# Kernel tuning notes

Measured on AMD Instinct MI355X. Metric: run time of the kernel, lower is better.

Reference implementation:

```python
import jax, jax.numpy as jnp
import numpy as np

B, L, D_MODEL, N_HEADS = 2, 2048, 2048, 16
HEAD_DIM = D_MODEL // N_HEADS
EPS = 1e-6
ROPE_THETA = 10000.0


def rms_norm(x, scale):
    # normalize over head_dim, learnable per-dim scale (QKNorm)
    var = jnp.mean(jnp.square(x), axis=-1, keepdims=True)
    return x * jax.lax.rsqrt(var + EPS) * scale


def rope(x, offset=0):
    # x: [B, H, T, D]; rotate-half rotary embedding over flattened positions
    T, D = x.shape[-2], x.shape[-1]
    half = D // 2
    inv_freq = 1.0 / (ROPE_THETA ** (jnp.arange(0, half, dtype=jnp.float32) / half))
    pos = jnp.arange(T, dtype=jnp.float32) + offset
    ang = pos[:, None] * inv_freq[None, :]            # [T, half]
    cos, sin = jnp.cos(ang), jnp.sin(ang)
    x1, x2 = x[..., :half], x[..., half:]
    return jnp.concatenate([x1 * cos - x2 * sin, x1 * sin + x2 * cos], axis=-1)


def setup_inputs() -> dict:
    key = jax.random.key(0)
    ks = jax.random.split(key, 7)
    s = 1.0 / np.sqrt(D_MODEL)
    x = jax.random.normal(ks[0], (B, L, D_MODEL), dtype=jnp.float32)
    w_qkv = jax.random.uniform(ks[1], (D_MODEL, 3 * D_MODEL), jnp.float32, -s, s)
    b_qkv = jax.random.uniform(ks[2], (3 * D_MODEL,), jnp.float32, -s, s)
    q_scale = jnp.ones((HEAD_DIM,), jnp.float32)
    k_scale = jnp.ones((HEAD_DIM,), jnp.float32)
    w_out = jax.random.uniform(ks[3], (D_MODEL, D_MODEL), jnp.float32, -s, s)
    b_out = jax.random.uniform(ks[4], (D_MODEL,), jnp.float32, -s, s)
    mask = jnp.tril(jnp.ones((L, L), dtype=bool))   # causal block mask pattern
    return {"x": x, "w_qkv": w_qkv, "b_qkv": b_qkv, "q_scale": q_scale,
            "k_scale": k_scale, "w_out": w_out, "b_out": b_out, "mask": mask}


def reference(x, w_qkv, b_qkv, q_scale, k_scale, w_out, b_out, mask):
    b, t, _ = x.shape
    qkv = x @ w_qkv + b_qkv                                   # [B, T, 3*D]
    qkv = qkv.reshape(b, t, 3, N_HEADS, HEAD_DIM)
    q, k, v = jnp.moveaxis(qkv, 2, 0)                          # each [B, T, H, D]
    q = jnp.transpose(q, (0, 2, 1, 3))                         # [B, H, T, D]
    k = jnp.transpose(k, (0, 2, 1, 3))
    v = jnp.transpose(v, (0, 2, 1, 3))
    q = rms_norm(q, q_scale)
    k = rms_norm(k, k_scale)
    q = rope(q, offset=0)
    k = rope(k, offset=0)
    scores = jnp.einsum('bhqd,bhkd->bhqk', q, k) / np.sqrt(HEAD_DIM)
    scores = jnp.where(mask[None, None, :, :], scores, jnp.float32(-1e30))
    attn = jax.nn.softmax(scores, axis=-1)
    out = jnp.einsum('bhqk,bhkd->bhqd', attn, v)               # [B, H, T, D]
    out = jnp.transpose(out, (0, 2, 1, 3)).reshape(b, t, D_MODEL)
    return out @ w_out + b_out
```

## Files before the change

### kernel.cpp

```cpp
#include <hip/hip_runtime.h>
#include <hip/hip_bf16.h>
#include <stdint.h>


typedef unsigned short ushort8 __attribute__((ext_vector_type(8)));
typedef unsigned short ushort4v __attribute__((ext_vector_type(4)));
typedef short          bf16x8 __attribute__((ext_vector_type(8)));
typedef float          f32x4  __attribute__((ext_vector_type(4)));

#define B_   2
#define L_   2048
#define DM   2048
#define NH   16
#define HD   128
#define QKW  4096

__device__ __forceinline__ uint16_t f2bf(float f){
  uint32_t u = __builtin_bit_cast(uint32_t, f);
  u += 0x7FFFu + ((u >> 16) & 1u);
  return (uint16_t)(u >> 16);
}
__device__ __forceinline__ float bf2f(uint16_t h){
  uint32_t u = ((uint32_t)h) << 16;
  return __builtin_bit_cast(float, u);
}

#define GLD16(gp, lp) __builtin_amdgcn_global_load_lds( \
  (const __attribute__((address_space(1))) void*)(gp),  \
  (__attribute__((address_space(3))) void*)(lp), 16, 0, 0)

__global__ __launch_bounds__(256) void rope_table(float* __restrict__ ct, float* __restrict__ st){
  int i = blockIdx.x * 256 + threadIdx.x;
  int t = i >> 6, d = i & 63;
  float invf = powf(10000.f, -(float)d * (1.f/64.f));
  float s, c;
  sincosf((float)t * invf, &s, &c);
  ct[i] = c; st[i] = s;
}

__global__ __launch_bounds__(256) void cvt_f32_bf16(const float* __restrict__ x,
                                                    uint16_t* __restrict__ o, int n8){
  int i = blockIdx.x * 256 + threadIdx.x;
  if (i < n8){
    const float4* xv = (const float4*)x;
    float4 a = xv[(size_t)i*2], b = xv[(size_t)i*2+1];
    ushort8 v;
    v[0]=f2bf(a.x); v[1]=f2bf(a.y); v[2]=f2bf(a.z); v[3]=f2bf(a.w);
    v[4]=f2bf(b.x); v[5]=f2bf(b.y); v[6]=f2bf(b.z); v[7]=f2bf(b.w);
    *(ushort8*)(o + (size_t)i*8) = v;
  }
}

__global__ __launch_bounds__(256) void transpose_w(const float* __restrict__ W,
                                                   uint16_t* __restrict__ Wt, int R, int C){
  __shared__ float T[64][65];
  const int rb = blockIdx.x, cb = blockIdx.y;
  const int tid = threadIdx.x;
#pragma unroll
  for (int i=0;i<4;i++){
    int rr = i*16 + (tid >> 4);
    int cc = (tid & 15) * 4;
    float4 v = *(const float4*)(W + (size_t)(rb*64 + rr) * C + cb*64 + cc);
    T[rr][cc] = v.x; T[rr][cc+1] = v.y; T[rr][cc+2] = v.z; T[rr][cc+3] = v.w;
  }
  __syncthreads();
  const int oc = tid >> 2, rc = (tid & 3) * 16;
  ushort8 o0, o1;
#pragma unroll
  for (int j=0;j<8;j++){ o0[j] = f2bf(T[rc+j][oc]); o1[j] = f2bf(T[rc+8+j][oc]); }
  size_t ob = (size_t)(cb*64 + oc) * R + rb*64 + rc;
  *(ushort8*)(Wt + ob)     = o0;
  *(ushort8*)(Wt + ob + 8) = o1;
}

template<int MODE>
__global__ __launch_bounds__(512, 2) void gemm8p(
    const uint16_t* __restrict__ A, const uint16_t* __restrict__ Bt,
    const float* __restrict__ bias, void* __restrict__ Cv, void* __restrict__ Cv2,
    int M, int N, int K, int nbn, int ldc,
    const float* __restrict__ qs, const float* __restrict__ ks,
    const float* __restrict__ ct, const float* __restrict__ st)
{
  __shared__ uint16_t LA[3*16384];
  __shared__ uint16_t LB[3*8192];
  __shared__ float sums[4][2][64];
  const int nwg = (M >> 8) * nbn;
  const int q8  = nwg >> 3;
  const int id  = ((int)blockIdx.x & 7) * q8 + ((int)blockIdx.x >> 3);
  const int bm = id / nbn, bn = id % nbn;
  const int tid = threadIdx.x;
  const int lane = tid & 63, w = tid >> 6;
  const int wm = w & 3, wn = w >> 2;
  const int l15 = lane & 15, lh = lane >> 4;
  const int NT = K >> 6;

  const int qs3 = ((lane & 7) ^ ((lane >> 3) & 7)) * 8;
  const uint16_t* gA_ = A  + (size_t)((bm << 8) + (w << 5) + (lane >> 3)) * K + qs3;
  const uint16_t* gB_ = Bt + (size_t)((bn << 7) + (w << 4) + (lane >> 3)) * K + qs3;
  uint16_t* lA_ = LA + (w << 11);
  uint16_t* lB_ = LB + (w << 10);

  const int sw0 = ((lh       ^ (l15 & 7)) << 3);
  const int sw1 = (((4 | lh) ^ (l15 & 7)) << 3);
  const int aoff = (((wm << 6) + l15) << 6);
  const int boff = (((wn << 5) + l15) << 6);
  const int bno[4] = {0, 1024, 4096, 5120};

  f32x4 acc[4][4];
#pragma unroll
  for (int i=0;i<4;i++)
#pragma unroll
    for (int j=0;j<4;j++) acc[i][j] = f32x4{0.f,0.f,0.f,0.f};

  auto STAGE_A = [&](int tt, int s, int i){
    GLD16(gA_ + (size_t)tt*64 + (size_t)(i*8)*K, lA_ + s*16384 + i*512);
  };
  auto STAGE_B = [&](int tt, int s, int i){
    GLD16(gB_ + (size_t)tt*64 + (size_t)(i*8)*K, lB_ + s*8192 + i*512);
  };

#pragma unroll
  for (int i=0;i<4;i++) STAGE_A(0, 0, i);
#pragma unroll
  for (int i=0;i<2;i++) STAGE_B(0, 0, i);
#pragma unroll
  for (int i=0;i<4;i++) STAGE_A(1, 1, i);
#pragma unroll
  for (int i=0;i<2;i++) STAGE_B(1, 1, i);
  asm volatile("s_waitcnt vmcnt(6)" ::: "memory");
  __builtin_amdgcn_s_barrier();

  int sl = 0, sl2 = 2;
  for (int t = 0; t < NT; ++t){
    const bool pf = (t + 2 < NT);
    const uint16_t* la = LA + sl*16384;
    const uint16_t* lb = LB + sl*8192;

    bf16x8 af0[4], bf0[4], af1[4], bf1[4];
#pragma unroll
    for (int mi=0;mi<4;mi++) af0[mi] = *(const bf16x8*)(la + aoff + mi*1024 + sw0);
#pragma unroll
    for (int ni=0;ni<4;ni++) bf0[ni] = *(const bf16x8*)(lb + boff + bno[ni] + sw0);
#pragma unroll
    for (int mi=0;mi<4;mi++) af1[mi] = *(const bf16x8*)(la + aoff + mi*1024 + sw1);
#pragma unroll
    for (int ni=0;ni<4;ni++) bf1[ni] = *(const bf16x8*)(lb + boff + bno[ni] + sw1);
    if (pf){
      STAGE_A(t+2, sl2, 0); STAGE_A(t+2, sl2, 1);
      STAGE_A(t+2, sl2, 2); STAGE_A(t+2, sl2, 3);
      STAGE_B(t+2, sl2, 0); STAGE_B(t+2, sl2, 1);
    }
    __builtin_amdgcn_s_setprio(1);
#pragma unroll
    for (int mi=0;mi<4;mi++)
#pragma unroll
      for (int ni=0;ni<4;ni++)
        acc[mi][ni] = __builtin_amdgcn_mfma_f32_16x16x32_bf16(af0[mi], bf0[ni], acc[mi][ni], 0, 0, 0);
#pragma unroll
    for (int mi=0;mi<4;mi++)
#pragma unroll
      for (int ni=0;ni<4;ni++)
        acc[mi][ni] = __builtin_amdgcn_mfma_f32_16x16x32_bf16(af1[mi], bf1[ni], acc[mi][ni], 0, 0, 0);
    __builtin_amdgcn_s_setprio(0);

    if (t < NT-2)       { asm volatile("s_waitcnt vmcnt(6)" ::: "memory"); }
    else if (t == NT-2) { asm volatile("s_waitcnt vmcnt(0)" ::: "memory"); }
    if (t < NT-1) __builtin_amdgcn_s_barrier();
    sl  = (sl  == 2) ? 0 : sl  + 1;
    sl2 = (sl2 == 2) ? 0 : sl2 + 1;
  }

  const int cm = (bm << 8) + (wm << 6);
  const int cn = (bn << 7);
  int dc[4];
#pragma unroll
  for (int ni=0;ni<4;ni++) dc[ni] = (wn<<5) + ((ni>>1)<<6) + ((ni&1)<<4) + l15;
  float bs[4];
#pragma unroll
  for (int ni=0;ni<4;ni++) bs[ni] = bias[cn + dc[ni]];

  if (MODE == 0){
#pragma unroll
    for (int mi=0;mi<4;mi++)
#pragma unroll
      for (int r=0;r<4;r++){
        int rowg = cm + mi*16 + lh*4 + r;
#pragma unroll
        for (int ni=0;ni<4;ni++)
          ((float*)Cv)[(size_t)rowg * ldc + cn + dc[ni]] = acc[mi][ni][r] + bs[ni];
      }
  } else {
    const int part = bn >> 4;
    if (part == 2){
      uint16_t* vtp = (uint16_t*)Cv2;
      const int h  = bn & 15;
      const int bb = cm >> 11;
      const int t0 = (cm & (L_-1)) + lh*4;
#pragma unroll
      for (int mi=0;mi<4;mi++){
#pragma unroll
        for (int ni=0;ni<4;ni++){
          ushort4v pk;
#pragma unroll
          for (int r=0;r<4;r++) pk[r] = f2bf(acc[mi][ni][r] + bs[ni]);
          *(ushort4v*)(vtp + ((size_t)((bb*16 + h)*128 + dc[ni]))*L_ + t0 + mi*16) = pk;
        }
      }
    } else {
      uint16_t* Cb = (uint16_t*)Cv;
      const float* scp = part ? ks : qs;
      float scv[4];
#pragma unroll
      for (int ni=0;ni<4;ni++) scv[ni] = scp[dc[ni]];
      float ssum[4][4];
#pragma unroll
      for (int mi=0;mi<4;mi++)
#pragma unroll
        for (int r=0;r<4;r++){
          float s = 0.f;
#pragma unroll
          for (int ni=0;ni<4;ni++){
            float v = acc[mi][ni][r] + bs[ni];
            acc[mi][ni][r] = v;
            s += v*v;
          }
          s += __shfl_xor(s, 1); s += __shfl_xor(s, 2);
          s += __shfl_xor(s, 4); s += __shfl_xor(s, 8);
          ssum[mi][r] = s;
        }
      if (l15 == 0){
#pragma unroll
        for (int mi=0;mi<4;mi++)
#pragma unroll
          for (int r=0;r<4;r++) sums[wm][wn][mi*16 + lh*4 + r] = ssum[mi][r];
      }
      __syncthreads();
      const int dd0 = (wn<<5) + l15, dd1 = dd0 + 16;
#pragma unroll
      for (int mi=0;mi<4;mi++){
#pragma unroll
        for (int r=0;r<4;r++){
          int rid = mi*16 + lh*4 + r;
          float tot = ssum[mi][r] + sums[wm][wn^1][rid];
          float iv = rsqrtf(tot * 0.0078125f + 1e-6f);
          int rowg = cm + rid;
          int t = rowg & (L_-1);
          float y0 = acc[mi][0][r] * iv * scv[0];
          float y1 = acc[mi][1][r] * iv * scv[1];
          float y2 = acc[mi][2][r] * iv * scv[2];
          float y3 = acc[mi][3][r] * iv * scv[3];
          float c0 = ct[t*64 + dd0], s0 = st[t*64 + dd0];
          float c1 = ct[t*64 + dd1], s1 = st[t*64 + dd1];
          size_t rb_ = (size_t)rowg * ldc + cn;
          Cb[rb_ + dc[0]] = f2bf(y0*c0 - y2*s0);
          Cb[rb_ + dc[1]] = f2bf(y1*c1 - y3*s1);
          Cb[rb_ + dc[2]] = f2bf(y0*s0 + y2*c0);
          Cb[rb_ + dc[3]] = f2bf(y1*s1 + y3*c1);
        }
      }
    }
  }
}

__global__ __launch_bounds__(256) void flash_attn(
    const uint16_t* __restrict__ qk, const uint16_t* __restrict__ vt,
    uint16_t* __restrict__ ao)
{
  const int qp = blockIdx.x;
  const int bh = blockIdx.y;
  const int b = bh >> 4, h = bh & 15;
  const int tid = threadIdx.x;
  const int lane = tid & 63, w = tid >> 6;
  const int l15 = lane & 15, lh = lane >> 4;

  __shared__ uint16_t Ks[64][136];
  __shared__ uint16_t Vs[128][72];
  __shared__ uint16_t Ps[4][16][72];

  const float SCL = 0.12751744f;

  for (int sel = 0; sel < 2; sel++){
    const int qb = sel ? (31 - qp) : qp;

    const size_t qrow = (size_t)b * L_ + qb*64 + w*16 + l15;
    const uint16_t* qp_ = qk + qrow * QKW + h * HD;
    bf16x8 qf[4];
#pragma unroll
    for (int c = 0; c < 4; c++) qf[c] = *(const bf16x8*)(qp_ + c*32 + lh*8);

    float m_s = -3.0e38f, l_s = 0.f;
    f32x4 oacc[8];
#pragma unroll
    for (int nt = 0; nt < 8; nt++) oacc[nt] = f32x4{0.f,0.f,0.f,0.f};

    const int ntile = qb + 1;
    ushort8 rk[4], rv[4];

#pragma unroll
    for (int i = 0; i < 4; i++){
      int g = i*256 + tid, row = g >> 4, c = g & 15;
      rk[i] = *(const ushort8*)(qk + ((size_t)b*L_ + row)*QKW + DM + h*HD + c*8);
    }
#pragma unroll
    for (int i = 0; i < 4; i++){
      int g = i*256 + tid, d = g >> 3, c = g & 7;
      rv[i] = *(const ushort8*)(vt + ((size_t)bh*HD + d)*L_ + c*8);
    }

    for (int kt = 0; kt < ntile; kt++){
      __syncthreads();
#pragma unroll
      for (int i = 0; i < 4; i++){ int g = i*256+tid; *(ushort8*)(&Ks[g>>4][(g&15)*8]) = rk[i]; }
#pragma unroll
      for (int i = 0; i < 4; i++){ int g = i*256+tid; *(ushort8*)(&Vs[g>>3][(g&7)*8]) = rv[i]; }
      __syncthreads();

      if (kt + 1 < ntile){
        const int k2 = (kt + 1) * 64;
#pragma unroll
        for (int i = 0; i < 4; i++){
          int g = i*256 + tid, row = g >> 4, c = g & 15;
          rk[i] = *(const ushort8*)(qk + ((size_t)b*L_ + k2 + row)*QKW + DM + h*HD + c*8);
        }
#pragma unroll
        for (int i = 0; i < 4; i++){
          int g = i*256 + tid, d = g >> 3, c = g & 7;
          rv[i] = *(const ushort8*)(vt + ((size_t)bh*HD + d)*L_ + k2 + c*8);
        }
      }

      f32x4 s[4];
#pragma unroll
      for (int nt = 0; nt < 4; nt++) s[nt] = f32x4{0.f,0.f,0.f,0.f};
      __builtin_amdgcn_s_setprio(1);
#pragma unroll
      for (int c = 0; c < 4; c++){
#pragma unroll
        for (int nt = 0; nt < 4; nt++){
          bf16x8 kf = *(const bf16x8*)(&Ks[nt*16 + l15][c*32 + lh*8]);
          s[nt] = __builtin_amdgcn_mfma_f32_16x16x32_bf16(kf, qf[c], s[nt], 0, 0, 0);
        }
      }
      __builtin_amdgcn_s_setprio(0);

      const bool diag = (kt == qb);
      const int qg = w*16 + l15;
      const int kb = lh*4;
#pragma unroll
      for (int nt = 0; nt < 4; nt++){
#pragma unroll
        for (int r = 0; r < 4; r++){
          float v = s[nt][r] * SCL;
          if (diag && (nt*16 + kb + r > qg)) v = -1.0e30f;
          s[nt][r] = v;
        }
      }
      float pm = s[0][0];
#pragma unroll
      for (int nt = 0; nt < 4; nt++)
#pragma unroll
        for (int r = 0; r < 4; r++) pm = fmaxf(pm, s[nt][r]);
      pm = fmaxf(pm, __shfl_xor(pm, 16));
      pm = fmaxf(pm, __shfl_xor(pm, 32));
      if (!__all(pm - m_s <= 8.0f)){
        float mn = fmaxf(m_s, pm);
        float alpha = exp2f(m_s - mn);
        m_s = mn; l_s *= alpha;
        float ar[4];
#pragma unroll
        for (int r = 0; r < 4; r++) ar[r] = __shfl(alpha, lh*4 + r);
#pragma unroll
        for (int nt = 0; nt < 8; nt++)
#pragma unroll
          for (int r = 0; r < 4; r++) oacc[nt][r] *= ar[r];
      }
      float rs = 0.f;
#pragma unroll
      for (int nt = 0; nt < 4; nt++){
        float p0 = exp2f(s[nt][0] - m_s);
        float p1 = exp2f(s[nt][1] - m_s);
        float p2 = exp2f(s[nt][2] - m_s);
        float p3 = exp2f(s[nt][3] - m_s);
        rs += (p0 + p1) + (p2 + p3);
        uint2 pk;
        pk.x = (uint32_t)f2bf(p0) | ((uint32_t)f2bf(p1) << 16);
        pk.y = (uint32_t)f2bf(p2) | ((uint32_t)f2bf(p3) << 16);
        *(uint2*)(&Ps[w][l15][nt*16 + kb]) = pk;
      }
      rs += __shfl_xor(rs, 16);
      rs += __shfl_xor(rs, 32);
      l_s += rs;

      asm volatile("s_waitcnt lgkmcnt(0)" ::: "memory");
      __builtin_amdgcn_s_setprio(1);
#pragma unroll
      for (int kc = 0; kc < 2; kc++){
        bf16x8 pf = *(const bf16x8*)(&Ps[w][l15][kc*32 + lh*8]);
#pragma unroll
        for (int nt = 0; nt < 8; nt++){
          bf16x8 vf = *(const bf16x8*)(&Vs[nt*16 + l15][kc*32 + lh*8]);
          oacc[nt] = __builtin_amdgcn_mfma_f32_16x16x32_bf16(pf, vf, oacc[nt], 0, 0, 0);
        }
      }
      __builtin_amdgcn_s_setprio(0);
    }
    float invl[4];
#pragma unroll
    for (int r = 0; r < 4; r++) invl[r] = 1.f / __shfl(l_s, lh*4 + r);
#pragma unroll
    for (int nt = 0; nt < 8; nt++){
#pragma unroll
      for (int r = 0; r < 4; r++){
        float v = oacc[nt][r] * invl[r];
        size_t row = (size_t)b*L_ + qb*64 + w*16 + lh*4 + r;
        ao[row * DM + h*HD + nt*16 + l15] = f2bf(v);
      }
    }
  }
}

extern "C" void kernel_launch(void* const* d_in, const int* in_sizes, int n_in,
                              void* d_out, int out_size, void* d_ws, size_t ws_size,
                              hipStream_t stream)
{
  (void)in_sizes; (void)n_in; (void)out_size; (void)ws_size;
  const float* x       = (const float*)d_in[0];
  const float* w_qkv   = (const float*)d_in[1];
  const float* b_qkv   = (const float*)d_in[2];
  const float* q_scale = (const float*)d_in[3];
  const float* k_scale = (const float*)d_in[4];
  const float* w_out   = (const float*)d_in[5];
  const float* b_out   = (const float*)d_in[6];
  float* out = (float*)d_out;

  char* ws = (char*)d_ws;
  uint16_t* qk    = (uint16_t*)(ws);
  uint16_t* vt    = (uint16_t*)(ws + 33554432);
  uint16_t* reg1  = (uint16_t*)(ws + 50331648);
  uint16_t* wqkvT = (uint16_t*)(ws + 67108864);
  uint16_t* woutT = (uint16_t*)(ws + 92274688);
  float*    ct    = (float*)(ws + 100663296);
  float*    st    = ct + 131072;

  uint16_t* xb = reg1;
  uint16_t* ao = reg1;

  rope_table  <<<512, 256, 0, stream>>>(ct, st);
  cvt_f32_bf16<<<4096, 256, 0, stream>>>(x, xb, 1048576);
  transpose_w <<<dim3(32, 96), 256, 0, stream>>>(w_qkv, wqkvT, 2048, 6144);
  transpose_w <<<dim3(32, 32), 256, 0, stream>>>(w_out, woutT, 2048, 2048);
  gemm8p<1>   <<<768, 512, 0, stream>>>(xb, wqkvT, b_qkv, qk, vt,
                                        4096, 6144, 2048, 48, 4096,
                                        q_scale, k_scale, ct, st);
  flash_attn  <<<dim3(16, 32), 256, 0, stream>>>(qk, vt, ao);
  gemm8p<0>   <<<256, 512, 0, stream>>>(ao, woutT, b_out, out, nullptr,
                                        4096, 2048, 2048, 16, 2048,
                                        nullptr, nullptr, nullptr, nullptr);
}
```

Baseline: 266.8 us.

## Split QKV GEMM into dedicated K=32-step kernel with higher occupancy

Replaces the templated QKV GEMM with a dedicated kernel that stages K in 32-wide slices. This halves LDS use per block and raises launch bounds to 4 blocks per CU, aiming to improve latency hiding through occupancy. The output-projection GEMM is simplified to a plain fp32 epilogue with contiguous 64-column warp tiles and no bno remapping. The trade-off is twice as many barriers and loop iterations per K in the QKV kernel, and possibly lower MFMA density per sync.

After: 287.9 us. 7.9% more time.

```diff
diff --git a/kernel.cpp b/kernel.cpp
--- a/kernel.cpp
+++ b/kernel.cpp
@@ -73,17 +73,166 @@
   *(ushort8*)(Wt + ob + 8) = o1;
 }
 
-template<int MODE>
-__global__ __launch_bounds__(512, 2) void gemm8p(
+__global__ __launch_bounds__(512, 4) void gemm32qkv(
     const uint16_t* __restrict__ A, const uint16_t* __restrict__ Bt,
-    const float* __restrict__ bias, void* __restrict__ Cv, void* __restrict__ Cv2,
-    int M, int N, int K, int nbn, int ldc,
+    const float* __restrict__ bias, uint16_t* __restrict__ qkOut,
+    uint16_t* __restrict__ vtOut,
     const float* __restrict__ qs, const float* __restrict__ ks,
     const float* __restrict__ ct, const float* __restrict__ st)
 {
+  constexpr int Mv = 4096, Nv = 6144, Kv = 2048, nbn = 48;
+  __shared__ uint16_t LA[3*8192];
+  __shared__ uint16_t LB[3*4096];
+  __shared__ float sums[4][2][64];
+  const int nwg = (Mv >> 8) * nbn;
+  const int q8  = nwg >> 3;
+  const int id  = ((int)blockIdx.x & 7) * q8 + ((int)blockIdx.x >> 3);
+  const int bm = id / nbn, bn = id % nbn;
+  const int tid = threadIdx.x;
+  const int lane = tid & 63, w = tid >> 6;
+  const int wm = w & 3, wn = w >> 2;
+  const int l15 = lane & 15, lh = lane >> 4;
+  const int NT = Kv >> 5;
+
+  const int qs3 = ((lane & 3) ^ ((lane >> 2) & 3)) * 8;
+  const uint16_t* gA_ = A  + (size_t)((bm << 8) + (w << 5) + (lane >> 2)) * Kv + qs3;
+  const uint16_t* gB_ = Bt + (size_t)((bn << 7) + (w << 4) + (lane >> 2)) * Kv + qs3;
+  uint16_t* lA_ = LA + (w << 10);
+  uint16_t* lB_ = LB + (w << 9);
+
+  const int swc = ((lh ^ (l15 & 3)) << 3);
+  const int aoff = (((wm << 6) + l15) << 5);
+  const int boff = (((wn << 5) + l15) << 5);
+  const int bno[4] = {0, 512, 2048, 2560};
+
+  f32x4 acc[4][4];
+#pragma unroll
+  for (int i=0;i<4;i++)
+#pragma unroll
+    for (int j=0;j<4;j++) acc[i][j] = f32x4{0.f,0.f,0.f,0.f};
+
+  auto STAGE = [&](int tt, int s){
+    GLD16(gA_ + (size_t)tt*32,               lA_ + s*8192);
+    GLD16(gA_ + (size_t)tt*32 + (size_t)16*Kv, lA_ + s*8192 + 512);
+    GLD16(gB_ + (size_t)tt*32,               lB_ + s*4096);
+  };
+
+  STAGE(0, 0); STAGE(1, 1);
+  asm volatile("s_waitcnt vmcnt(3)" ::: "memory");
+  __builtin_amdgcn_s_barrier();
+
+  int sl = 0, sl2 = 2;
+  for (int t = 0; t < NT; ++t){
+    const uint16_t* la = LA + sl*8192;
+    const uint16_t* lb = LB + sl*4096;
+
+    bf16x8 af[4], bf[4];
+#pragma unroll
+    for (int mi=0;mi<4;mi++) af[mi] = *(const bf16x8*)(la + aoff + mi*512 + swc);
+#pragma unroll
+    for (int ni=0;ni<4;ni++) bf[ni] = *(const bf16x8*)(lb + boff + bno[ni] + swc);
+    if (t + 2 < NT) STAGE(t+2, sl2);
+
+    __builtin_amdgcn_s_setprio(1);
+#pragma unroll
+    for (int mi=0;mi<4;mi++)
+#pragma unroll
+      for (int ni=0;ni<4;ni++)
+        acc[mi][ni] = __builtin_amdgcn_mfma_f32_16x16x32_bf16(af[mi], bf[ni], acc[mi][ni], 0, 0, 0);
+    __builtin_amdgcn_s_setprio(0);
+
+    if (t < NT-2)       { asm volatile("s_waitcnt vmcnt(3)" ::: "memory"); }
+    else if (t == NT-2) { asm volatile("s_waitcnt vmcnt(0)" ::: "memory"); }
+    if (t < NT-1) __builtin_amdgcn_s_barrier();
+    sl  = (sl  == 2) ? 0 : sl  + 1;
+    sl2 = (sl2 == 2) ? 0 : sl2 + 1;
+  }
+
+  const int cm = (bm << 8) + (wm << 6);
+  const int cn = (bn << 7);
+  int dc[4];
+#pragma unroll
+  for (int ni=0;ni<4;ni++) dc[ni] = (wn<<5) + ((ni>>1)<<6) + ((ni&1)<<4) + l15;
+  float bs[4];
+#pragma unroll
+  for (int ni=0;ni<4;ni++) bs[ni] = bias[cn + dc[ni]];
+
+  const int part = bn >> 4;
+  if (part == 2){
+    const int h  = bn & 15;
+    const int bb = cm >> 11;
+    const int t0 = (cm & (L_-1)) + lh*4;
+#pragma unroll
+    for (int mi=0;mi<4;mi++){
+#pragma unroll
+      for (int ni=0;ni<4;ni++){
+        ushort4v pk;
+#pragma unroll
+        for (int r=0;r<4;r++) pk[r] = f2bf(acc[mi][ni][r] + bs[ni]);
+        *(ushort4v*)(vtOut + ((size_t)((bb*16 + h)*128 + dc[ni]))*L_ + t0 + mi*16) = pk;
+      }
+    }
+  } else {
+    const float* scp = part ? ks : qs;
+    float scv[4];
+#pragma unroll
+    for (int ni=0;ni<4;ni++) scv[ni] = scp[dc[ni]];
+    float ssum[4][4];
+#pragma unroll
+    for (int mi=0;mi<4;mi++)
+#pragma unroll
+      for (int r=0;r<4;r++){
+        float s = 0.f;
+#pragma unroll
+        for (int ni=0;ni<4;ni++){
+          float v = acc[mi][ni][r] + bs[ni];
+          acc[mi][ni][r] = v;
+          s += v*v;
+        }
+        s += __shfl_xor(s, 1); s += __shfl_xor(s, 2);
+        s += __shfl_xor(s, 4); s += __shfl_xor(s, 8);
+        ssum[mi][r] = s;
+      }
+    if (l15 == 0){
+#pragma unroll
+      for (int mi=0;mi<4;mi++)
+#pragma unroll
+        for (int r=0;r<4;r++) sums[wm][wn][mi*16 + lh*4 + r] = ssum[mi][r];
+    }
+    __syncthreads();
+    const int dd0 = (wn<<5) + l15, dd1 = dd0 + 16;
+#pragma unroll
+    for (int mi=0;mi<4;mi++){
+#pragma unroll
+      for (int r=0;r<4;r++){
+        int rid = mi*16 + lh*4 + r;
+        float tot = ssum[mi][r] + sums[wm][wn^1][rid];
+        float iv = rsqrtf(tot * 0.0078125f + 1e-6f);
+        int rowg = cm + rid;
+        int t = rowg & (L_-1);
+        float y0 = acc[mi][0][r] * iv * scv[0];
+        float y1 = acc[mi][1][r] * iv * scv[1];
+        float y2 = acc[mi][2][r] * iv * scv[2];
+        float y3 = acc[mi][3][r] * iv * scv[3];
+        float c0 = ct[t*64 + dd0], s0 = st[t*64 + dd0];
+        float c1 = ct[t*64 + dd1], s1 = st[t*64 + dd1];
+        size_t rb_ = (size_t)rowg * QKW + cn;
+        qkOut[rb_ + dc[0]] = f2bf(y0*c0 - y2*s0);
+        qkOut[rb_ + dc[1]] = f2bf(y1*c1 - y3*s1);
+        qkOut[rb_ + dc[2]] = f2bf(y0*s0 + y2*c0);
+        qkOut[rb_ + dc[3]] = f2bf(y1*s1 + y3*c1);
+      }
+    }
+  }
+}
+
+__global__ __launch_bounds__(512, 2) void gemm8p(
+    const uint16_t* __restrict__ A, const uint16_t* __restrict__ Bt,
+    const float* __restrict__ bias, float* __restrict__ Cv,
+    int M, int N, int K, int nbn)
+{
   __shared__ uint16_t LA[3*16384];
   __shared__ uint16_t LB[3*8192];
-  __shared__ float sums[4][2][64];
   const int nwg = (M >> 8) * nbn;
   const int q8  = nwg >> 3;
   const int id  = ((int)blockIdx.x & 7) * q8 + ((int)blockIdx.x >> 3);
@@ -103,8 +252,7 @@
   const int sw0 = ((lh       ^ (l15 & 7)) << 3);
   const int sw1 = (((4 | lh) ^ (l15 & 7)) << 3);
   const int aoff = (((wm << 6) + l15) << 6);
-  const int boff = (((wn << 5) + l15) << 6);
-  const int bno[4] = {0, 1024, 4096, 5120};
+  const int boff = (((wn << 6) + l15) << 6);
 
   f32x4 acc[4][4];
 #pragma unroll
@@ -140,11 +288,11 @@
 #pragma unroll
     for (int mi=0;mi<4;mi++) af0[mi] = *(const bf16x8*)(la + aoff + mi*1024 + sw0);
 #pragma unroll
-    for (int ni=0;ni<4;ni++) bf0[ni] = *(const bf16x8*)(lb + boff + bno[ni] + sw0);
+    for (int ni=0;ni<4;ni++) bf0[ni] = *(const bf16x8*)(lb + boff + ni*1024 + sw0);
 #pragma unroll
     for (int mi=0;mi<4;mi++) af1[mi] = *(const bf16x8*)(la + aoff + mi*1024 + sw1);
 #pragma unroll
-    for (int ni=0;ni<4;ni++) bf1[ni] = *(const bf16x8*)(lb + boff + bno[ni] + sw1);
+    for (int ni=0;ni<4;ni++) bf1[ni] = *(const bf16x8*)(lb + boff + ni*1024 + sw1);
     if (pf){
       STAGE_A(t+2, sl2, 0); STAGE_A(t+2, sl2, 1);
       STAGE_A(t+2, sl2, 2); STAGE_A(t+2, sl2, 3);
@@ -171,92 +319,17 @@
   }
 
   const int cm = (bm << 8) + (wm << 6);
-  const int cn = (bn << 7);
-  int dc[4];
-#pragma unroll
-  for (int ni=0;ni<4;ni++) dc[ni] = (wn<<5) + ((ni>>1)<<6) + ((ni&1)<<4) + l15;
-  float bs[4];
-#pragma unroll
-  for (int ni=0;ni<4;ni++) bs[ni] = bias[cn + dc[ni]];
-
-  if (MODE == 0){
-#pragma unroll
-    for (int mi=0;mi<4;mi++)
+  const int cn = (bn << 7) + (wn << 6);
+#pragma unroll
+  for (int ni=0;ni<4;ni++){
+    int col = cn + ni*16 + l15;
+    float bs = bias[col];
+#pragma unroll
+    for (int mi=0;mi<4;mi++){
 #pragma unroll
       for (int r=0;r<4;r++){
         int rowg = cm + mi*16 + lh*4 + r;
-#pragma unroll
-        for (int ni=0;ni<4;ni++)
-          ((float*)Cv)[(size_t)rowg * ldc + cn + dc[ni]] = acc[mi][ni][r] + bs[ni];
-      }
-  } else {
-    const int part = bn >> 4;
-    if (part == 2){
-      uint16_t* vtp = (uint16_t*)Cv2;
-      const int h  = bn & 15;
-      const int bb = cm >> 11;
-      const int t0 = (cm & (L_-1)) + lh*4;
-#pragma unroll
-      for (int mi=0;mi<4;mi++){
-#pragma unroll
-        for (int ni=0;ni<4;ni++){
-          ushort4v pk;
-#pragma unroll
-          for (int r=0;r<4;r++) pk[r] = f2bf(acc[mi][ni][r] + bs[ni]);
-          *(ushort4v*)(vtp + ((size_t)((bb*16 + h)*128 + dc[ni]))*L_ + t0 + mi*16) = pk;
-        }
-      }
-    } else {
-      uint16_t* Cb = (uint16_t*)Cv;
-      const float* scp = part ? ks : qs;
-      float scv[4];
-#pragma unroll
-      for (int ni=0;ni<4;ni++) scv[ni] = scp[dc[ni]];
-      float ssum[4][4];
-#pragma unroll
-      for (int mi=0;mi<4;mi++)
-#pragma unroll
-        for (int r=0;r<4;r++){
-          float s = 0.f;
-#pragma unroll
-          for (int ni=0;ni<4;ni++){
-            float v = acc[mi][ni][r] + bs[ni];
-            acc[mi][ni][r] = v;
-            s += v*v;
-          }
-          s += __shfl_xor(s, 1); s += __shfl_xor(s, 2);
-          s += __shfl_xor(s, 4); s += __shfl_xor(s, 8);
-          ssum[mi][r] = s;
-        }
-      if (l15 == 0){
-#pragma unroll
-        for (int mi=0;mi<4;mi++)
-#pragma unroll
-          for (int r=0;r<4;r++) sums[wm][wn][mi*16 + lh*4 + r] = ssum[mi][r];
-      }
-      __syncthreads();
-      const int dd0 = (wn<<5) + l15, dd1 = dd0 + 16;
-#pragma unroll
-      for (int mi=0;mi<4;mi++){
-#pragma unroll
-        for (int r=0;r<4;r++){
-          int rid = mi*16 + lh*4 + r;
-          float tot = ssum[mi][r] + sums[wm][wn^1][rid];
-          float iv = rsqrtf(tot * 0.0078125f + 1e-6f);
-          int rowg = cm + rid;
-          int t = rowg & (L_-1);
-          float y0 = acc[mi][0][r] * iv * scv[0];
-          float y1 = acc[mi][1][r] * iv * scv[1];
-          float y2 = acc[mi][2][r] * iv * scv[2];
-          float y3 = acc[mi][3][r] * iv * scv[3];
-          float c0 = ct[t*64 + dd0], s0 = st[t*64 + dd0];
-          float c1 = ct[t*64 + dd1], s1 = st[t*64 + dd1];
-          size_t rb_ = (size_t)rowg * ldc + cn;
-          Cb[rb_ + dc[0]] = f2bf(y0*c0 - y2*s0);
-          Cb[rb_ + dc[1]] = f2bf(y1*c1 - y3*s1);
-          Cb[rb_ + dc[2]] = f2bf(y0*s0 + y2*c0);
-          Cb[rb_ + dc[3]] = f2bf(y1*s1 + y3*c1);
-        }
+        Cv[(size_t)rowg * N + col] = acc[mi][ni][r] + bs;
       }
     }
   }
@@ -449,11 +522,8 @@
   cvt_f32_bf16<<<4096, 256, 0, stream>>>(x, xb, 1048576);
   transpose_w <<<dim3(32, 96), 256, 0, stream>>>(w_qkv, wqkvT, 2048, 6144);
   transpose_w <<<dim3(32, 32), 256, 0, stream>>>(w_out, woutT, 2048, 2048);
-  gemm8p<1>   <<<768, 512, 0, stream>>>(xb, wqkvT, b_qkv, qk, vt,
-                                        4096, 6144, 2048, 48, 4096,
+  gemm32qkv   <<<768, 512, 0, stream>>>(xb, wqkvT, b_qkv, qk, vt,
                                         q_scale, k_scale, ct, st);
   flash_attn  <<<dim3(16, 32), 256, 0, stream>>>(qk, vt, ao);
-  gemm8p<0>   <<<256, 512, 0, stream>>>(ao, woutT, b_out, out, nullptr,
-                                        4096, 2048, 2048, 16, 2048,
-                                        nullptr, nullptr, nullptr, nullptr);
-}
+  gemm8p      <<<256, 512, 0, stream>>>(ao, woutT, b_out, out, 4096, 2048, 2048, 16);
+}
```
